# Kernel tuning notes

Hardware: AMD Instinct MI355X
Metric: run time of the kernel (lower is better)

## Reference

```python
import jax, jax.numpy as jnp
import numpy as np

LN_EPS = 1e-12


def setup_inputs() -> dict:
    key = jax.random.key(0)
    ks = jax.random.split(key, 5)
    B, N, D_IN, D_OUT, E = 32, 2048, 128, 128, 64
    return {
        "x": jax.random.normal(ks[0], (B, N, D_IN), dtype=jnp.float32),
        "node_embeddings": jax.random.normal(ks[1], (N, E), dtype=jnp.float32),
        "time_embeddings": jax.random.normal(ks[2], (E,), dtype=jnp.float32),
        "weights_pool": jax.random.normal(ks[3], (E, 2, D_IN, D_OUT), dtype=jnp.float32) * 0.02,
        "bias_pool": jax.random.normal(ks[4], (E, D_OUT), dtype=jnp.float32) * 0.02,
        "ln_weight": jnp.ones((E,), dtype=jnp.float32),
        "ln_bias": jnp.zeros((E,), dtype=jnp.float32),
    }


def reference(x, node_embeddings, time_embeddings, weights_pool, bias_pool, ln_weight, ln_bias):
    # e: [N, E] = LayerNorm(node_emb + time_emb)  (dropout in eval mode = identity)
    e = node_embeddings + time_embeddings[None, :]
    mu = jnp.mean(e, axis=-1, keepdims=True)
    var = jnp.mean(jnp.square(e - mu), axis=-1, keepdims=True)
    e = (e - mu) * jax.lax.rsqrt(var + LN_EPS) * ln_weight + ln_bias

    # adaptive adjacency: softmax over rows of e @ e.T  -> [N, N]
    adj = jax.nn.softmax(jnp.einsum('nd,md->nm', e, e), axis=1)

    # per-node weights [N, 2, I, O] and bias [N, O]
    weights = jnp.einsum('nd,dkio->nkio', e, weights_pool)
    bias = e @ bias_pool  # [N, O]

    # supports: k=0 identity (x itself), k=1 adjacency aggregation
    x_agg = jnp.einsum('nm,bmc->bnc', adj, x)        # [B, N, I]
    x_g = jnp.stack([x, x_agg], axis=2)              # [B, N, 2, I]

    # per-node batched GEMM + bias
    out = jnp.einsum('bnki,nkio->bno', x_g, weights) + bias
    return out
```

## Files before the change

kernel.cpp:

```cpp
#include <hip/hip_runtime.h>


typedef unsigned short u16;
typedef unsigned int u32;
typedef __attribute__((ext_vector_type(8))) short bf16x8;
typedef __attribute__((ext_vector_type(4))) float f32x4;

#define NN 2048
#define EE 64
#define CC 128
#define BB 32

__device__ __forceinline__ u16 f2bf(float f) {
  u32 u = __builtin_bit_cast(u32, f);
  u += 0x7fffu + ((u >> 16) & 1u);
  return (u16)(u >> 16);
}

__device__ __forceinline__ f32x4 mfma16(bf16x8 a, bf16x8 b, f32x4 c) {
  return __builtin_amdgcn_mfma_f32_16x16x32_bf16(a, b, c, 0, 0, 0);
}

__global__ __launch_bounds__(64) void k_prep(
    const float* __restrict__ ne, const float* __restrict__ te,
    const float* __restrict__ lnw, const float* __restrict__ lnb,
    const float* __restrict__ bias_pool,
    float* __restrict__ e, u16* __restrict__ e_bf, float* __restrict__ bias_out) {
  int n = blockIdx.x;
  int d = threadIdx.x;
  float v = ne[n * EE + d] + te[d];
  float s = v;
#pragma unroll
  for (int off = 32; off > 0; off >>= 1) s += __shfl_xor(s, off);
  float mean = s * (1.0f / 64.0f);
  float c = v - mean;
  float q = c * c;
#pragma unroll
  for (int off = 32; off > 0; off >>= 1) q += __shfl_xor(q, off);
  float inv = rsqrtf(q * (1.0f / 64.0f) + 1e-12f);
  float ev = c * inv * lnw[d] + lnb[d];
  e[n * EE + d] = ev;
  e_bf[n * EE + d] = f2bf(ev);
  __shared__ float sh[64];
  sh[d] = ev;
  __syncthreads();
#pragma unroll
  for (int oo = 0; oo < 2; ++oo) {
    int o = oo * 64 + d;
    float acc = 0.f;
#pragma unroll 8
    for (int dd = 0; dd < 64; ++dd) acc += sh[dd] * bias_pool[dd * CC + o];
    bias_out[n * CC + o] = acc;
  }
}

__global__ __launch_bounds__(256) void k_poolt(const float* __restrict__ pool,
                                               u16* __restrict__ pool_t) {
  __shared__ float t[128 * 65];
  int ki = blockIdx.x;
  int tid = threadIdx.x;
  for (int it = 0; it < 32; ++it) {
    int idx = it * 256 + tid;
    int d = idx >> 7, o = idx & 127;
    t[o * 65 + d] = pool[d * 32768 + ki * 128 + o];
  }
  __syncthreads();
  for (int it = 0; it < 32; ++it) {
    int idx = it * 256 + tid;
    int o = idx >> 6, d = idx & 63;
    pool_t[ki * 8192 + o * 64 + d] = f2bf(t[o * 65 + d]);
  }
}

__global__ __launch_bounds__(256) void k_xtrans(const float* __restrict__ x,
                                                u16* __restrict__ x_t,
                                                u16* __restrict__ x_bf) {
  __shared__ u16 t[128 * 68];
  int b = blockIdx.x >> 5;
  int m0 = (blockIdx.x & 31) * 64;
  int tid = threadIdx.x;
  for (int it = 0; it < 32; ++it) {
    int idx = it * 256 + tid;
    int m = idx >> 7, c = idx & 127;
    float v = x[(b * NN + m0 + m) * CC + c];
    u16 h = f2bf(v);
    x_bf[(b * NN + m0 + m) * CC + c] = h;
    t[c * 68 + m] = h;
  }
  __syncthreads();
  for (int it = 0; it < 32; ++it) {
    int idx = it * 256 + tid;
    int c = idx >> 6, m = idx & 63;
    x_t[(b * CC + c) * NN + m0 + m] = t[c * 68 + m];
  }
}

__global__ __launch_bounds__(256) void k_S(const float* __restrict__ e,
                                           float* __restrict__ S) {
  extern __shared__ float sm[];
  float* er = sm;
  float* ec = sm + 128 * 68;
  int n0 = (blockIdx.x >> 4) * 128, m0 = (blockIdx.x & 15) * 128;
  int tid = threadIdx.x;
  for (int it = 0; it < 32; ++it) {
    int idx = it * 256 + tid;
    int r = idx >> 6, d = idx & 63;
    er[r * 68 + d] = e[(n0 + r) * EE + d];
    ec[r * 68 + d] = e[(m0 + r) * EE + d];
  }
  __syncthreads();
  int tx = tid & 15, ty = tid >> 4;
  float acc[8][8] = {};
  for (int d4 = 0; d4 < 64; d4 += 4) {
    f32x4 av[8], bv[8];
#pragma unroll
    for (int i = 0; i < 8; ++i) av[i] = *(const f32x4*)&er[(ty + 16 * i) * 68 + d4];
#pragma unroll
    for (int j = 0; j < 8; ++j) bv[j] = *(const f32x4*)&ec[(tx + 16 * j) * 68 + d4];
#pragma unroll
    for (int i = 0; i < 8; ++i)
#pragma unroll
      for (int j = 0; j < 8; ++j) {
        acc[i][j] += av[i][0] * bv[j][0];
        acc[i][j] += av[i][1] * bv[j][1];
        acc[i][j] += av[i][2] * bv[j][2];
        acc[i][j] += av[i][3] * bv[j][3];
      }
  }
#pragma unroll
  for (int i = 0; i < 8; ++i)
#pragma unroll
    for (int j = 0; j < 8; ++j)
      S[(n0 + ty + 16 * i) * NN + m0 + tx + 16 * j] = acc[i][j];
}

__global__ __launch_bounds__(256) void k_softmax(const float* __restrict__ S,
                                                 u16* __restrict__ adj) {
  int n = blockIdx.x;
  int tid = threadIdx.x;
  int lane = tid & 63, w = tid >> 6;
  __shared__ float red[8];
  const f32x4* Srow = (const f32x4*)(S + (size_t)n * NN);
  f32x4 v0 = Srow[tid];
  f32x4 v1 = Srow[256 + tid];
  float mx = v0[0];
#pragma unroll
  for (int k = 1; k < 4; ++k) mx = fmaxf(mx, v0[k]);
#pragma unroll
  for (int k = 0; k < 4; ++k) mx = fmaxf(mx, v1[k]);
#pragma unroll
  for (int off = 32; off > 0; off >>= 1) mx = fmaxf(mx, __shfl_xor(mx, off));
  if (lane == 0) red[w] = mx;
  __syncthreads();
  mx = fmaxf(fmaxf(red[0], red[1]), fmaxf(red[2], red[3]));
  float ex[8];
  float sum = 0.f;
#pragma unroll
  for (int k = 0; k < 4; ++k) { ex[k] = __expf(v0[k] - mx); sum += ex[k]; }
#pragma unroll
  for (int k = 0; k < 4; ++k) { ex[4 + k] = __expf(v1[k] - mx); sum += ex[4 + k]; }
#pragma unroll
  for (int off = 32; off > 0; off >>= 1) sum += __shfl_xor(sum, off);
  if (lane == 0) red[4 + w] = sum;
  __syncthreads();
  sum = red[4] + red[5] + red[6] + red[7];
  float rs = 1.0f / sum;
  u16* arow = adj + (size_t)n * NN;
  u32 p0 = (u32)f2bf(ex[0] * rs) | ((u32)f2bf(ex[1] * rs) << 16);
  u32 p1 = (u32)f2bf(ex[2] * rs) | ((u32)f2bf(ex[3] * rs) << 16);
  ((uint2*)arow)[tid] = make_uint2(p0, p1);
  p0 = (u32)f2bf(ex[4] * rs) | ((u32)f2bf(ex[5] * rs) << 16);
  p1 = (u32)f2bf(ex[6] * rs) | ((u32)f2bf(ex[7] * rs) << 16);
  ((uint2*)arow)[256 + tid] = make_uint2(p0, p1);
}

__global__ __launch_bounds__(256) void k_aggr(const u16* __restrict__ adj,
                                              const u16* __restrict__ x_t,
                                              u16* __restrict__ xagg) {
  __shared__ u16 As[128 * 72];
  __shared__ u16 Bs[128 * 72];
  int mb = blockIdx.x & 15, b = blockIdx.x >> 4;
  int n0 = mb * 128;
  int tid = threadIdx.x;
  int lane = tid & 63, w = tid >> 6;
  int wm = w >> 1, wn = w & 1;
  int lm = lane & 15, lq = lane >> 4;
  f32x4 acc[4][4] = {};
  const u16* a_src = adj + (size_t)n0 * NN;
  const u16* b_src = x_t + (size_t)b * CC * NN;
  for (int kc = 0; kc < NN; kc += 64) {
    __syncthreads();
#pragma unroll
    for (int ii = 0; ii < 4; ++ii) {
      int idx = ii * 256 + tid;
      int row = idx >> 3, ch = idx & 7;
      *(bf16x8*)&As[row * 72 + ch * 8] = *(const bf16x8*)&a_src[(size_t)row * NN + kc + ch * 8];
      *(bf16x8*)&Bs[row * 72 + ch * 8] = *(const bf16x8*)&b_src[(size_t)row * NN + kc + ch * 8];
    }
    __syncthreads();
#pragma unroll
    for (int kk = 0; kk < 64; kk += 32) {
      bf16x8 af[4], bq[4];
#pragma unroll
      for (int i = 0; i < 4; ++i)
        af[i] = *(const bf16x8*)&As[(wm * 64 + i * 16 + lm) * 72 + kk + lq * 8];
#pragma unroll
      for (int j = 0; j < 4; ++j)
        bq[j] = *(const bf16x8*)&Bs[(wn * 64 + j * 16 + lm) * 72 + kk + lq * 8];
#pragma unroll
      for (int i = 0; i < 4; ++i)
#pragma unroll
        for (int j = 0; j < 4; ++j)
          acc[i][j] = mfma16(af[i], bq[j], acc[i][j]);
    }
  }
#pragma unroll
  for (int i = 0; i < 4; ++i) {
    int nr = n0 + wm * 64 + i * 16 + lq * 4;
#pragma unroll
    for (int j = 0; j < 4; ++j) {
      int c = wn * 64 + j * 16 + lm;
#pragma unroll
      for (int r = 0; r < 4; ++r)
        xagg[((size_t)b * NN + nr + r) * CC + c] = f2bf(acc[i][j][r]);
    }
  }
}

__global__ __launch_bounds__(256) void k_out(const u16* __restrict__ e_bf,
                                             const u16* __restrict__ pool_t,
                                             const u16* __restrict__ x_bf,
                                             const u16* __restrict__ xagg,
                                             const float* __restrict__ bias,
                                             float* __restrict__ out) {
  extern __shared__ u16 Wl[];
  int og = blockIdx.x >> 7, ng = blockIdx.x & 127;
  int n0 = ng * 16, o0 = og * 16;
  int tid = threadIdx.x;
  int lane = tid & 63, w = tid >> 6;
  int lm = lane & 15, lq = lane >> 4;
  bf16x8 a0 = *(const bf16x8*)&e_bf[(n0 + lm) * EE + lq * 8];
  bf16x8 a1 = *(const bf16x8*)&e_bf[(n0 + lm) * EE + 32 + lq * 8];
#pragma unroll 4
  for (int t = 0; t < 64; ++t) {
    int ki = w * 64 + t;
    const u16* bp = pool_t + ((size_t)ki * 128 + o0 + lm) * 64 + lq * 8;
    bf16x8 b0 = *(const bf16x8*)bp;
    bf16x8 b1 = *(const bf16x8*)(bp + 32);
    f32x4 acc = {0.f, 0.f, 0.f, 0.f};
    acc = mfma16(a0, b0, acc);
    acc = mfma16(a1, b1, acc);
#pragma unroll
    for (int r = 0; r < 4; ++r) {
      int nd = lq * 4 + r;
      Wl[(nd * 16 + lm) * 264 + ki] = f2bf(acc[r]);
    }
  }
  __syncthreads();
#pragma unroll
  for (int nn = 0; nn < 4; ++nn) {
    int ndl = w * 4 + nn;
    int n = n0 + ndl;
    f32x4 acc0 = {0.f, 0.f, 0.f, 0.f}, acc1 = {0.f, 0.f, 0.f, 0.f};
#pragma unroll
    for (int ks = 0; ks < 8; ++ks) {
      int ki = ks * 32 + lq * 8;
      bf16x8 av0, av1;
      if (ks < 4) {
        av0 = *(const bf16x8*)&x_bf[((size_t)lm * NN + n) * CC + ki];
        av1 = *(const bf16x8*)&x_bf[(((size_t)16 + lm) * NN + n) * CC + ki];
      } else {
        av0 = *(const bf16x8*)&xagg[((size_t)lm * NN + n) * CC + ki - 128];
        av1 = *(const bf16x8*)&xagg[(((size_t)16 + lm) * NN + n) * CC + ki - 128];
      }
      bf16x8 bv = *(const bf16x8*)&Wl[(ndl * 16 + lm) * 264 + ki];
      acc0 = mfma16(av0, bv, acc0);
      acc1 = mfma16(av1, bv, acc1);
    }
    float bvv = bias[n * CC + o0 + lm];
#pragma unroll
    for (int r = 0; r < 4; ++r) {
      int br = lq * 4 + r;
      out[((size_t)br * NN + n) * CC + o0 + lm] = acc0[r] + bvv;
      out[(((size_t)16 + br) * NN + n) * CC + o0 + lm] = acc1[r] + bvv;
    }
  }
}

extern "C" void kernel_launch(void* const* d_in, const int* in_sizes, int n_in,
                              void* d_out, int out_size, void* d_ws, size_t ws_size,
                              hipStream_t stream) {
  const float* x        = (const float*)d_in[0];
  const float* node_emb = (const float*)d_in[1];
  const float* time_emb = (const float*)d_in[2];
  const float* pool     = (const float*)d_in[3];
  const float* bias_pl  = (const float*)d_in[4];
  const float* ln_w     = (const float*)d_in[5];
  const float* ln_b     = (const float*)d_in[6];
  float* out = (float*)d_out;

  char* p = (char*)d_ws;
  auto alloc = [&](size_t bytes) {
    char* r = p;
    p += (bytes + 255) & ~(size_t)255;
    return r;
  };
  float* e      = (float*)alloc((size_t)NN * EE * 4);
  u16*   e_bf   = (u16*)  alloc((size_t)NN * EE * 2);
  float* biasb  = (float*)alloc((size_t)NN * CC * 4);
  u16*   adj    = (u16*)  alloc((size_t)NN * NN * 2);
  u16*   x_t    = (u16*)  alloc((size_t)BB * CC * NN * 2);
  u16*   x_bf   = (u16*)  alloc((size_t)BB * NN * CC * 2);
  u16*   pool_t = (u16*)  alloc((size_t)256 * 128 * 64 * 2);
  char*  Sx     = alloc((size_t)NN * NN * 4);
  float* S      = (float*)Sx;
  u16*   xagg   = (u16*)Sx;

  if (ws_size < (size_t)(p - (char*)d_ws)) return;

  (void)hipFuncSetAttribute((const void*)k_S, hipFuncAttributeMaxDynamicSharedMemorySize,
                            2 * 128 * 68 * 4);
  (void)hipFuncSetAttribute((const void*)k_out, hipFuncAttributeMaxDynamicSharedMemorySize,
                            16 * 16 * 264 * 2);

  k_prep<<<NN, 64, 0, stream>>>(node_emb, time_emb, ln_w, ln_b, bias_pl, e, e_bf, biasb);
  k_poolt<<<256, 256, 0, stream>>>(pool, pool_t);
  k_xtrans<<<BB * 32, 256, 0, stream>>>(x, x_t, x_bf);
  k_S<<<256, 256, 2 * 128 * 68 * 4, stream>>>(e, S);
  k_softmax<<<NN, 256, 0, stream>>>(S, adj);
  k_aggr<<<16 * BB, 256, 0, stream>>>(adj, x_t, xagg);
  k_out<<<8 * 128, 256, 16 * 16 * 264 * 2, stream>>>(e_bf, pool_t, x_bf, xagg, biasb, out);
}
```

Measured before the change: 267.3 us.

## Restructure k_out to chunk K with streamed per-node weights and wider output tiles

Measured after the change: 253.8 us. 5.1% less time.

```diff
diff --git a/kernel.cpp b/kernel.cpp
--- a/kernel.cpp
+++ b/kernel.cpp
@@ -55,7 +55,7 @@
 }
 
 __global__ __launch_bounds__(256) void k_poolt(const float* __restrict__ pool,
-                                               u16* __restrict__ pool_t) {
+                                               u16* __restrict__ pool_r) {
   __shared__ float t[128 * 65];
   int ki = blockIdx.x;
   int tid = threadIdx.x;
@@ -68,7 +68,7 @@
   for (int it = 0; it < 32; ++it) {
     int idx = it * 256 + tid;
     int o = idx >> 6, d = idx & 63;
-    pool_t[ki * 8192 + o * 64 + d] = f2bf(t[o * 65 + d]);
+    pool_r[((size_t)o * 256 + ki) * 64 + d] = f2bf(t[o * 65 + d]);
   }
 }
 
@@ -227,62 +227,73 @@
   }
 }
 
-__global__ __launch_bounds__(256) void k_out(const u16* __restrict__ e_bf,
-                                             const u16* __restrict__ pool_t,
-                                             const u16* __restrict__ x_bf,
-                                             const u16* __restrict__ xagg,
-                                             const float* __restrict__ bias,
-                                             float* __restrict__ out) {
-  extern __shared__ u16 Wl[];
-  int og = blockIdx.x >> 7, ng = blockIdx.x & 127;
-  int n0 = ng * 16, o0 = og * 16;
+#define WL_OS 36
+#define WL_NS 1192
+__global__ __launch_bounds__(512, 4) void k_out(const u16* __restrict__ e_bf,
+                                                const u16* __restrict__ pool_r,
+                                                const u16* __restrict__ x_bf,
+                                                const u16* __restrict__ xagg,
+                                                const float* __restrict__ bias,
+                                                float* __restrict__ out) {
+  __shared__ u16 Wl[16 * WL_NS];
+  int ng = blockIdx.x & 127, og = blockIdx.x >> 7;
+  int n0 = ng * 16, o0 = og * 32;
   int tid = threadIdx.x;
   int lane = tid & 63, w = tid >> 6;
   int lm = lane & 15, lq = lane >> 4;
-  bf16x8 a0 = *(const bf16x8*)&e_bf[(n0 + lm) * EE + lq * 8];
-  bf16x8 a1 = *(const bf16x8*)&e_bf[(n0 + lm) * EE + 32 + lq * 8];
-#pragma unroll 4
-  for (int t = 0; t < 64; ++t) {
-    int ki = w * 64 + t;
-    const u16* bp = pool_t + ((size_t)ki * 128 + o0 + lm) * 64 + lq * 8;
-    bf16x8 b0 = *(const bf16x8*)bp;
-    bf16x8 b1 = *(const bf16x8*)(bp + 32);
-    f32x4 acc = {0.f, 0.f, 0.f, 0.f};
-    acc = mfma16(a0, b0, acc);
-    acc = mfma16(a1, b1, acc);
-#pragma unroll
-    for (int r = 0; r < 4; ++r) {
-      int nd = lq * 4 + r;
-      Wl[(nd * 16 + lm) * 264 + ki] = f2bf(acc[r]);
-    }
-  }
-  __syncthreads();
-#pragma unroll
-  for (int nn = 0; nn < 4; ++nn) {
-    int ndl = w * 4 + nn;
-    int n = n0 + ndl;
-    f32x4 acc0 = {0.f, 0.f, 0.f, 0.f}, acc1 = {0.f, 0.f, 0.f, 0.f};
-#pragma unroll
-    for (int ks = 0; ks < 8; ++ks) {
-      int ki = ks * 32 + lq * 8;
-      bf16x8 av0, av1;
-      if (ks < 4) {
-        av0 = *(const bf16x8*)&x_bf[((size_t)lm * NN + n) * CC + ki];
-        av1 = *(const bf16x8*)&x_bf[(((size_t)16 + lm) * NN + n) * CC + ki];
-      } else {
-        av0 = *(const bf16x8*)&xagg[((size_t)lm * NN + n) * CC + ki - 128];
-        av1 = *(const bf16x8*)&xagg[(((size_t)16 + lm) * NN + n) * CC + ki - 128];
+  bf16x8 e0 = *(const bf16x8*)&e_bf[(n0 + lm) * EE + lq * 8];
+  bf16x8 e1 = *(const bf16x8*)&e_bf[(n0 + lm) * EE + 32 + lq * 8];
+  f32x4 acc[2][2][2] = {};
+  for (int c = 0; c < 8; ++c) {
+#pragma unroll
+    for (int oi = 0; oi < 4; ++oi) {
+      int o = w * 4 + oi;
+#pragma unroll
+      for (int kh = 0; kh < 2; ++kh) {
+        const u16* ap = pool_r + ((size_t)(o0 + o) * 256 + c * 32 + kh * 16 + lm) * 64 + lq * 8;
+        bf16x8 p0 = *(const bf16x8*)ap;
+        bf16x8 p1 = *(const bf16x8*)(ap + 32);
+        f32x4 g = {0.f, 0.f, 0.f, 0.f};
+        g = mfma16(p0, e0, g);
+        g = mfma16(p1, e1, g);
+        ushort4 h;
+        h.x = f2bf(g[0]); h.y = f2bf(g[1]); h.z = f2bf(g[2]); h.w = f2bf(g[3]);
+        *(ushort4*)&Wl[lm * WL_NS + o * WL_OS + kh * 16 + lq * 4] = h;
       }
-      bf16x8 bv = *(const bf16x8*)&Wl[(ndl * 16 + lm) * 264 + ki];
-      acc0 = mfma16(av0, bv, acc0);
-      acc1 = mfma16(av1, bv, acc1);
-    }
-    float bvv = bias[n * CC + o0 + lm];
-#pragma unroll
-    for (int r = 0; r < 4; ++r) {
-      int br = lq * 4 + r;
-      out[((size_t)br * NN + n) * CC + o0 + lm] = acc0[r] + bvv;
-      out[(((size_t)16 + br) * NN + n) * CC + o0 + lm] = acc1[r] + bvv;
+    }
+    __syncthreads();
+#pragma unroll
+    for (int nn = 0; nn < 2; ++nn) {
+      int ndl = w * 2 + nn;
+      int n = n0 + ndl;
+      const u16* xs = (c < 4) ? x_bf : xagg;
+      int ck = (c < 4) ? c * 32 : c * 32 - 128;
+      bf16x8 a0 = *(const bf16x8*)&xs[((size_t)lm * NN + n) * CC + ck + lq * 8];
+      bf16x8 a1 = *(const bf16x8*)&xs[(((size_t)16 + lm) * NN + n) * CC + ck + lq * 8];
+#pragma unroll
+      for (int nt = 0; nt < 2; ++nt) {
+        bf16x8 bv = *(const bf16x8*)&Wl[ndl * WL_NS + (nt * 16 + lm) * WL_OS + lq * 8];
+        acc[nn][0][nt] = mfma16(a0, bv, acc[nn][0][nt]);
+        acc[nn][1][nt] = mfma16(a1, bv, acc[nn][1][nt]);
+      }
+    }
+    __syncthreads();
+  }
+#pragma unroll
+  for (int nn = 0; nn < 2; ++nn) {
+    int n = n0 + w * 2 + nn;
+#pragma unroll
+    for (int nt = 0; nt < 2; ++nt) {
+      int oc = o0 + nt * 16 + lm;
+      float bv = bias[n * CC + oc];
+#pragma unroll
+      for (int mt = 0; mt < 2; ++mt) {
+#pragma unroll
+        for (int r = 0; r < 4; ++r) {
+          int b = mt * 16 + lq * 4 + r;
+          out[((size_t)b * NN + n) * CC + oc] = acc[nn][mt][nt][r] + bv;
+        }
+      }
     }
   }
 }
@@ -311,7 +322,7 @@
   u16*   adj    = (u16*)  alloc((size_t)NN * NN * 2);
   u16*   x_t    = (u16*)  alloc((size_t)BB * CC * NN * 2);
   u16*   x_bf   = (u16*)  alloc((size_t)BB * NN * CC * 2);
-  u16*   pool_t = (u16*)  alloc((size_t)256 * 128 * 64 * 2);
+  u16*   pool_r = (u16*)  alloc((size_t)128 * 256 * 64 * 2);
   char*  Sx     = alloc((size_t)NN * NN * 4);
   float* S      = (float*)Sx;
   u16*   xagg   = (u16*)Sx;
@@ -320,14 +331,12 @@
 
   (void)hipFuncSetAttribute((const void*)k_S, hipFuncAttributeMaxDynamicSharedMemorySize,
                             2 * 128 * 68 * 4);
-  (void)hipFuncSetAttribute((const void*)k_out, hipFuncAttributeMaxDynamicSharedMemorySize,
-                            16 * 16 * 264 * 2);
 
   k_prep<<<NN, 64, 0, stream>>>(node_emb, time_emb, ln_w, ln_b, bias_pl, e, e_bf, biasb);
-  k_poolt<<<256, 256, 0, stream>>>(pool, pool_t);
+  k_poolt<<<256, 256, 0, stream>>>(pool, pool_r);
   k_xtrans<<<BB * 32, 256, 0, stream>>>(x, x_t, x_bf);
   k_S<<<256, 256, 2 * 128 * 68 * 4, stream>>>(e, S);
   k_softmax<<<NN, 256, 0, stream>>>(S, adj);
   k_aggr<<<16 * BB, 256, 0, stream>>>(adj, x_t, xagg);
-  k_out<<<8 * 128, 256, 16 * 16 * 264 * 2, stream>>>(e_bf, pool_t, x_bf, xagg, biasb, out);
-}
+  k_out<<<512, 512, 0, stream>>>(e_bf, pool_r, x_bf, xagg, biasb, out);
+}
```
